# Kernel tuning notes

Measured on AMD Instinct MI355X. Metric: run time of the kernel, lower is better.

## Reference

```python
import jax, jax.numpy as jnp
import numpy as np

B, S, D = 4, 2048, 1024
H, K = 16, 64
NUM_WINDOW = 8
LN_EPS = 1e-3  # keras LayerNormalization default epsilon


def _mha(x, Wq, bq, Wk, bk, Wv, bv, Wo, bo):
    # x: [b, s, D]; Wq/Wk/Wv: [D, H, K]; Wo: [H, K, D]
    q = jnp.einsum('bsd,dhk->bshk', x, Wq) + bq
    k = jnp.einsum('bsd,dhk->bshk', x, Wk) + bk
    v = jnp.einsum('bsd,dhk->bshk', x, Wv) + bv
    scores = jnp.einsum('bqhk,bshk->bhqs', q, k) / jnp.sqrt(jnp.asarray(K, q.dtype))
    attn = jax.nn.softmax(scores, axis=-1)
    o = jnp.einsum('bhqs,bshk->bqhk', attn, v)
    return jnp.einsum('bqhk,hkd->bqd', o, Wo) + bo


def setup_inputs() -> dict:
    key = jax.random.key(0)
    ks = jax.random.split(key, 20)
    sc = 0.02
    def proj(k):
        return jax.random.normal(k, (D, H, K), jnp.float32) * sc
    inp = {
        'x': jax.random.normal(ks[0], (B, S, D), jnp.float32),
        # global MHA params
        'gWq': proj(ks[1]), 'gbq': jnp.zeros((H, K), jnp.float32),
        'gWk': proj(ks[2]), 'gbk': jnp.zeros((H, K), jnp.float32),
        'gWv': proj(ks[3]), 'gbv': jnp.zeros((H, K), jnp.float32),
        'gWo': jax.random.normal(ks[4], (H, K, D), jnp.float32) * sc,
        'gbo': jnp.zeros((D,), jnp.float32),
        # local MHA params (shared across all windows)
        'lWq': proj(ks[5]), 'lbq': jnp.zeros((H, K), jnp.float32),
        'lWk': proj(ks[6]), 'lbk': jnp.zeros((H, K), jnp.float32),
        'lWv': proj(ks[7]), 'lbv': jnp.zeros((H, K), jnp.float32),
        'lWo': jax.random.normal(ks[8], (H, K, D), jnp.float32) * sc,
        'lbo': jnp.zeros((D,), jnp.float32),
        # layernorm params
        'gamma': jnp.ones((D,), jnp.float32),
        'beta': jnp.zeros((D,), jnp.float32),
    }
    return inp


def reference(x, gWq, gbq, gWk, gbk, gWv, gbv, gWo, gbo,
              lWq, lbq, lWk, lbk, lWv, lbv, lWo, lbo, gamma, beta):
    # global full self-attention
    g_out = _mha(x, gWq, gbq, gWk, gbk, gWv, gbv, gWo, gbo)
    # local windowed self-attention: split seq into NUM_WINDOW blocks; all
    # windows share the same local_mha weights, so fold windows into batch.
    w = S // NUM_WINDOW
    xw = x.reshape(B * NUM_WINDOW, w, D)
    l_out = _mha(xw, lWq, lbq, lWk, lbk, lWv, lbv, lWo, lbo).reshape(B, S, D)
    # residual add of all three streams, then layernorm
    y = x + g_out + l_out
    mu = jnp.mean(y, axis=-1, keepdims=True)
    var = jnp.mean(jnp.square(y - mu), axis=-1, keepdims=True)
    return (y - mu) * jax.lax.rsqrt(var + LN_EPS) * gamma + beta
```

## Files before the change

### kernel.cpp

```cpp
#include <hip/hip_runtime.h>
#include <hip/hip_bf16.h>
#include <type_traits>

using bf16 = __hip_bfloat16;
typedef __bf16 bf16x8 __attribute__((ext_vector_type(8)));
typedef float f32x4 __attribute__((ext_vector_type(4)));
typedef float f32x16 __attribute__((ext_vector_type(16)));
typedef unsigned short u16x8 __attribute__((ext_vector_type(8)));
typedef unsigned int u32;
typedef unsigned int u32x4 __attribute__((ext_vector_type(4)));

#define LOG2E 1.4426950408889634f

static __device__ __forceinline__ unsigned short f2bf_bits(float f) {
  bf16 h = __float2bfloat16(f);
  return __builtin_bit_cast(unsigned short, h);
}

__global__ __launch_bounds__(256) void wtr_kernel(const float* __restrict__ W,
                                                  bf16* __restrict__ out,
                                                  int out_ld, int r_off) {
  __shared__ float tile[32][33];
  int tx = threadIdx.x & 31, ty = threadIdx.x >> 5;
  int c0 = blockIdx.x * 32, r0 = blockIdx.y * 32;
#pragma unroll
  for (int i = 0; i < 4; ++i)
    tile[ty + i * 8][tx] = W[(size_t)(r0 + ty + i * 8) * 1024 + c0 + tx];
  __syncthreads();
#pragma unroll
  for (int i = 0; i < 4; ++i) {
    int cr = ty + i * 8;
    out[(size_t)(c0 + cr) * out_ld + r_off + r0 + tx] = __float2bfloat16(tile[tx][cr]);
  }
}

__global__ void biascat_kernel(const float* gbq, const float* gbk, const float* gbv,
                               const float* lbq, const float* lbk, const float* lbv,
                               const float* gbo, const float* lbo,
                               float* bqkv, float* bo) {
  int i = blockIdx.x * 256 + threadIdx.x;
  if (i < 1024) {
    bqkv[i] = gbq[i];
    bqkv[1024 + i] = gbk[i];
    bqkv[2048 + i] = gbv[i];
    bqkv[3072 + i] = lbq[i];
    bqkv[4096 + i] = lbk[i];
    bqkv[5120 + i] = lbv[i];
    bo[i] = gbo[i] + lbo[i];
  }
}

__global__ __launch_bounds__(256) void castx_kernel(const float* __restrict__ x,
                                                    unsigned short* __restrict__ xb) {
  size_t i = (size_t)blockIdx.x * 256 + threadIdx.x;
  float4 v = reinterpret_cast<const float4*>(x)[i];
  ushort4 o = make_ushort4(f2bf_bits(v.x), f2bf_bits(v.y), f2bf_bits(v.z), f2bf_bits(v.w));
  reinterpret_cast<ushort4*>(xb)[i] = o;
}

template <typename OutT>
__global__ __launch_bounds__(256) void gemm_bt_kernel(
    const bf16* __restrict__ A, const bf16* __restrict__ Bt,
    OutT* __restrict__ C, const float* __restrict__ bias,
    int M, int N, int Kd) {
  __shared__ unsigned short lA[128 * 64];
  __shared__ unsigned short lB[128 * 64];
  const int tid = threadIdx.x;
  const int lane = tid & 63;
  const int wv = tid >> 6;
  const int g = lane >> 4, r15 = lane & 15;
  const int nbx = N >> 7;
  const int nwg = gridDim.x;
  const int bid = blockIdx.x;
  const int wg = (bid & 7) * (nwg >> 3) + (bid >> 3);
  const int tR = (wg / nbx) << 7;
  const int tC = (wg % nbx) << 7;
  const int wr = wv >> 1, wc = wv & 1;

  f32x4 acc[4][4] = {};

  const int srow = lane >> 3;
  const int scol = ((lane & 7) ^ (lane >> 3)) << 3;

  const bf16* Ab = A + (size_t)tR * Kd;
  const bf16* Bb = Bt + (size_t)tC * Kd;

  const int nk = Kd >> 6;
  for (int kt = 0; kt < nk; ++kt) {
    const int k0 = kt << 6;
#pragma unroll
    for (int i = 0; i < 4; ++i) {
      const int c = i * 4 + wv;
      const bf16* gA = Ab + (size_t)(c * 8 + srow) * Kd + (k0 + scol);
      __builtin_amdgcn_global_load_lds(
          (const __attribute__((address_space(1))) unsigned int*)gA,
          (__attribute__((address_space(3))) unsigned int*)&lA[c * 512], 16, 0, 0);
      const bf16* gB = Bb + (size_t)(c * 8 + srow) * Kd + (k0 + scol);
      __builtin_amdgcn_global_load_lds(
          (const __attribute__((address_space(1))) unsigned int*)gB,
          (__attribute__((address_space(3))) unsigned int*)&lB[c * 512], 16, 0, 0);
    }
    __syncthreads();
#pragma unroll
    for (int kk = 0; kk < 2; ++kk) {
      bf16x8 af[4], bfr[4];
#pragma unroll
      for (int m = 0; m < 4; ++m) {
        int row = (wr << 6) + (m << 4) + r15;
        int byt = row * 128 + (((kk << 6) + (g << 4)) ^ ((row & 7) << 4));
        af[m] = *reinterpret_cast<const bf16x8*>((const char*)lA + byt);
      }
#pragma unroll
      for (int n = 0; n < 4; ++n) {
        int row = (wc << 6) + (n << 4) + r15;
        int byt = row * 128 + (((kk << 6) + (g << 4)) ^ ((row & 7) << 4));
        bfr[n] = *reinterpret_cast<const bf16x8*>((const char*)lB + byt);
      }
#pragma unroll
      for (int m = 0; m < 4; ++m)
#pragma unroll
        for (int n = 0; n < 4; ++n)
          acc[m][n] = __builtin_amdgcn_mfma_f32_16x16x32_bf16(af[m], bfr[n], acc[m][n], 0, 0, 0);
    }
    __syncthreads();
  }

#pragma unroll
  for (int n = 0; n < 4; ++n) {
    const int col = tC + (wc << 6) + (n << 4) + r15;
    const float bv = bias ? bias[col] : 0.0f;
#pragma unroll
    for (int m = 0; m < 4; ++m) {
      const int row0 = tR + (wr << 6) + (m << 4) + (g << 2);
#pragma unroll
      for (int j = 0; j < 4; ++j) {
        float v = acc[m][n][j] + bv;
        if constexpr (std::is_same<OutT, float>::value)
          C[(size_t)(row0 + j) * N + col] = v;
        else
          C[(size_t)(row0 + j) * N + col] = __float2bfloat16(v);
      }
    }
  }
}

__global__ __launch_bounds__(256) void vtr_kernel(const bf16* __restrict__ qkv,
                                                  bf16* __restrict__ vt, int colOff) {
  __shared__ unsigned short t[64][72];
  const int tid = threadIdx.x;
  const int s0 = blockIdx.x * 64, h = blockIdx.y, b = blockIdx.z;
  const int sr = tid >> 3, d0 = (tid & 7) * 8;
  const bf16* src = qkv + colOff + h * 64;
#pragma unroll
  for (int p = 0; p < 2; ++p) {
    int s = sr + p * 32;
    u16x8 v = *reinterpret_cast<const u16x8*>(src + (size_t)(b * 2048 + s0 + s) * 6144 + d0);
    *reinterpret_cast<u16x8*>(&t[s][d0]) = v;
  }
  __syncthreads();
  bf16* dst = vt + (size_t)((b * 16 + h) * 64) * 2048 + s0;
#pragma unroll
  for (int p = 0; p < 2; ++p) {
    int d = sr + p * 32;
    u16x8 o;
#pragma unroll
    for (int i = 0; i < 8; ++i) o[i] = t[d0 + i][d];
    *reinterpret_cast<u16x8*>(dst + (size_t)d * 2048 + d0) = o;
  }
}

__global__ __launch_bounds__(256, 3) void attn_kernel(
    const bf16* __restrict__ qkv, const bf16* __restrict__ vt,
    bf16* __restrict__ outp, int qOff, int kOff, int oOff, int isLocal) {
  __shared__ unsigned short lK[2][64 * 64];
  __shared__ unsigned short lV[2][64 * 64];
  const int ldq = 6144;
  const int tid = threadIdx.x, lane = tid & 63, wv = tid >> 6;
  const int q31 = lane & 31, hi = lane >> 5;
  const int qb = blockIdx.x, h = blockIdx.y, b = blockIdx.z;
  const int q0 = qb * 128 + wv * 32;

  const int srow = lane >> 3;
  const int scol = ((lane & 7) ^ (lane >> 3)) << 3;

  const bf16* qp = qkv + (size_t)(b * 2048 + q0 + q31) * ldq + qOff + h * 64 + hi * 8;
  bf16x8 qf0 = *reinterpret_cast<const bf16x8*>(qp);
  bf16x8 qf1 = *reinterpret_cast<const bf16x8*>(qp + 16);
  bf16x8 qf2 = *reinterpret_cast<const bf16x8*>(qp + 32);
  bf16x8 qf3 = *reinterpret_cast<const bf16x8*>(qp + 48);

  const int t0 = isLocal ? ((qb >> 1) << 2) : 0;
  const int nt = isLocal ? 4 : 32;

  const bf16* Kb = qkv + kOff + h * 64;
  const bf16* Vb = vt + (size_t)((b * 16 + h) * 64) * 2048;

  auto stage = [&](int t, int buf) {
    const int krow0 = b * 2048 + t * 64;
#pragma unroll
    for (int i = 0; i < 2; ++i) {
      const int c = i * 4 + wv;
      const int row = c * 8 + srow;
      const bf16* gK = Kb + (size_t)(krow0 + row) * ldq + scol;
      __builtin_amdgcn_global_load_lds(
          (const __attribute__((address_space(1))) unsigned int*)gK,
          (__attribute__((address_space(3))) unsigned int*)&lK[buf][c * 512], 16, 0, 0);
      const bf16* gV = Vb + (size_t)row * 2048 + t * 64 + scol;
      __builtin_amdgcn_global_load_lds(
          (const __attribute__((address_space(1))) unsigned int*)gV,
          (__attribute__((address_space(3))) unsigned int*)&lV[buf][c * 512], 16, 0, 0);
    }
  };

  float mrun = -1e30f, lrun = 0.f;
  f32x16 accO0 = {}, accO1 = {};
  const float C8 = 0.125f * LOG2E;

  stage(t0, 0);
  for (int tt = 0; tt < nt; ++tt) {
    const int buf = tt & 1;
    __syncthreads();
    if (tt + 1 < nt) stage(t0 + tt + 1, buf ^ 1);

    f32x16 s0 = {}, s1 = {};
    const char* lkb = (const char*)&lK[buf][0];
#pragma unroll
    for (int kap = 0; kap < 4; ++kap) {
      bf16x8 qf = kap == 0 ? qf0 : kap == 1 ? qf1 : kap == 2 ? qf2 : qf3;
      {
        const int row = q31;
        bf16x8 kf = *reinterpret_cast<const bf16x8*>(
            lkb + row * 128 + ((kap * 32 + hi * 16) ^ ((row & 7) << 4)));
        s0 = __builtin_amdgcn_mfma_f32_32x32x16_bf16(kf, qf, s0, 0, 0, 0);
      }
      {
        const int row = 32 + q31;
        bf16x8 kf = *reinterpret_cast<const bf16x8*>(
            lkb + row * 128 + ((kap * 32 + hi * 16) ^ ((row & 7) << 4)));
        s1 = __builtin_amdgcn_mfma_f32_32x32x16_bf16(kf, qf, s1, 0, 0, 0);
      }
    }

    float m2 = s0[0];
#pragma unroll
    for (int i = 1; i < 16; ++i) m2 = fmaxf(m2, s0[i]);
#pragma unroll
    for (int i = 0; i < 16; ++i) m2 = fmaxf(m2, s1[i]);
    m2 = fmaxf(m2, __shfl_xor(m2, 32));
    if (__any(m2 > mrun + 64.0f)) {
      float mn = fmaxf(mrun, m2);
      float ascl = exp2f((mrun - mn) * C8);
      mrun = mn;
      lrun *= ascl;
      accO0 *= ascl;
      accO1 *= ascl;
    }
    const float nm = -mrun * C8;
    float rs = 0.f;
#pragma unroll
    for (int i = 0; i < 16; ++i) { s0[i] = exp2f(fmaf(s0[i], C8, nm)); rs += s0[i]; }
#pragma unroll
    for (int i = 0; i < 16; ++i) { s1[i] = exp2f(fmaf(s1[i], C8, nm)); rs += s1[i]; }
    rs += __shfl_xor(rs, 32);
    lrun += rs;

    u32 W0[8], W1[8];
#pragma unroll
    for (int m = 0; m < 4; ++m)
#pragma unroll
      for (int u = 0; u < 2; ++u) {
        W0[m * 2 + u] = (u32)f2bf_bits(s0[m * 4 + 2 * u]) |
                        ((u32)f2bf_bits(s0[m * 4 + 2 * u + 1]) << 16);
        W1[m * 2 + u] = (u32)f2bf_bits(s1[m * 4 + 2 * u]) |
                        ((u32)f2bf_bits(s1[m * 4 + 2 * u + 1]) << 16);
      }

    const char* lvb = (const char*)&lV[buf][0];
#define PV_BLOCK(Wb, KAP)                                                          \
  {                                                                                \
    u32 w0 = Wb[(((KAP) & 1) * 2) * 2 + 0], w1 = Wb[(((KAP) & 1) * 2) * 2 + 1];    \
    u32 w2 = Wb[(((KAP) & 1) * 2 + 1) * 2 + 0], w3 = Wb[(((KAP) & 1) * 2 + 1) * 2 + 1]; \
    asm("v_permlane32_swap_b32 %0, %1" : "+v"(w0), "+v"(w2));                      \
    asm("v_permlane32_swap_b32 %0, %1" : "+v"(w1), "+v"(w3));                      \
    bf16x8 pa = __builtin_bit_cast(bf16x8, (u32x4){w0, w1, w2, w3});               \
    {                                                                              \
      const int row = q31;                                                         \
      bf16x8 vf = *reinterpret_cast<const bf16x8*>(                                \
          lvb + row * 128 + (((KAP) * 32 + hi * 16) ^ ((row & 7) << 4)));          \
      accO0 = __builtin_amdgcn_mfma_f32_32x32x16_bf16(vf, pa, accO0, 0, 0, 0);     \
    }                                                                              \
    {                                                                              \
      const int row = 32 + q31;                                                    \
      bf16x8 vf = *reinterpret_cast<const bf16x8*>(                                \
          lvb + row * 128 + (((KAP) * 32 + hi * 16) ^ ((row & 7) << 4)));          \
      accO1 = __builtin_amdgcn_mfma_f32_32x32x16_bf16(vf, pa, accO1, 0, 0, 0);     \
    }                                                                              \
  }
    PV_BLOCK(W0, 0)
    PV_BLOCK(W0, 1)
    PV_BLOCK(W1, 2)
    PV_BLOCK(W1, 3)
#undef PV_BLOCK
  }

  const float inv = 1.0f / lrun;
  bf16* orow = outp + (size_t)(b * 2048 + q0 + q31) * 2048 + oOff + h * 64;
#pragma unroll
  for (int rg = 0; rg < 4; ++rg) {
    const int d0 = 8 * rg + 4 * hi;
    ushort4 o0 = make_ushort4(f2bf_bits(accO0[4 * rg + 0] * inv), f2bf_bits(accO0[4 * rg + 1] * inv),
                              f2bf_bits(accO0[4 * rg + 2] * inv), f2bf_bits(accO0[4 * rg + 3] * inv));
    *reinterpret_cast<ushort4*>(orow + d0) = o0;
    ushort4 o1 = make_ushort4(f2bf_bits(accO1[4 * rg + 0] * inv), f2bf_bits(accO1[4 * rg + 1] * inv),
                              f2bf_bits(accO1[4 * rg + 2] * inv), f2bf_bits(accO1[4 * rg + 3] * inv));
    *reinterpret_cast<ushort4*>(orow + 32 + d0) = o1;
  }
}

__global__ __launch_bounds__(256) void ln_kernel(const float* __restrict__ x,
                                                 const float* __restrict__ ygl,
                                                 const float* __restrict__ gamma,
                                                 const float* __restrict__ beta,
                                                 float* __restrict__ out) {
  const int row = blockIdx.x, t = threadIdx.x, lane = t & 63, wv = t >> 6;
  __shared__ float red[8];
  const float4* xr = reinterpret_cast<const float4*>(x + (size_t)row * 1024);
  const float4* yr = reinterpret_cast<const float4*>(ygl + (size_t)row * 1024);
  float4 a = xr[t], c = yr[t];
  float y0 = a.x + c.x, y1 = a.y + c.y, y2 = a.z + c.z, y3 = a.w + c.w;
  float s = y0 + y1 + y2 + y3;
#pragma unroll
  for (int o = 32; o; o >>= 1) s += __shfl_down(s, o);
  if (!lane) red[wv] = s;
  __syncthreads();
  float mu = (red[0] + red[1] + red[2] + red[3]) * (1.f / 1024.f);
  float d0 = y0 - mu, d1 = y1 - mu, d2 = y2 - mu, d3 = y3 - mu;
  float q = d0 * d0 + d1 * d1 + d2 * d2 + d3 * d3;
#pragma unroll
  for (int o = 32; o; o >>= 1) q += __shfl_down(q, o);
  if (!lane) red[4 + wv] = q;
  __syncthreads();
  float var = (red[4] + red[5] + red[6] + red[7]) * (1.f / 1024.f);
  float r = rsqrtf(var + 1e-3f);
  float4 gm = reinterpret_cast<const float4*>(gamma)[t];
  float4 bt = reinterpret_cast<const float4*>(beta)[t];
  float4 o4;
  o4.x = d0 * r * gm.x + bt.x;
  o4.y = d1 * r * gm.y + bt.y;
  o4.z = d2 * r * gm.z + bt.z;
  o4.w = d3 * r * gm.w + bt.w;
  reinterpret_cast<float4*>(out + (size_t)row * 1024)[t] = o4;
}

extern "C" void kernel_launch(void* const* d_in, const int* in_sizes, int n_in,
                              void* d_out, int out_size, void* d_ws, size_t ws_size,
                              hipStream_t stream) {
  const float* x = (const float*)d_in[0];
  const float* gWq = (const float*)d_in[1];
  const float* gbq = (const float*)d_in[2];
  const float* gWk = (const float*)d_in[3];
  const float* gbk = (const float*)d_in[4];
  const float* gWv = (const float*)d_in[5];
  const float* gbv = (const float*)d_in[6];
  const float* gWo = (const float*)d_in[7];
  const float* gbo = (const float*)d_in[8];
  const float* lWq = (const float*)d_in[9];
  const float* lbq = (const float*)d_in[10];
  const float* lWk = (const float*)d_in[11];
  const float* lbk = (const float*)d_in[12];
  const float* lWv = (const float*)d_in[13];
  const float* lbv = (const float*)d_in[14];
  const float* lWo = (const float*)d_in[15];
  const float* lbo = (const float*)d_in[16];
  const float* gamma = (const float*)d_in[17];
  const float* beta = (const float*)d_in[18];
  float* out = (float*)d_out;

  char* ws = (char*)d_ws;
  size_t off = 0;
  auto alloc = [&](size_t bytes) {
    void* p = ws + off;
    off += (bytes + 255) & ~(size_t)255;
    return p;
  };
  bf16* xb = (bf16*)alloc((size_t)8192 * 1024 * 2);
  bf16* Wt = (bf16*)alloc((size_t)6144 * 1024 * 2);
  bf16* WoT = (bf16*)alloc((size_t)1024 * 2048 * 2);
  float* bQKV = (float*)alloc(6144 * 4);
  float* bO = (float*)alloc(1024 * 4);
  bf16* QKV = (bf16*)alloc((size_t)8192 * 6144 * 2);
  bf16* Vtg = (bf16*)alloc((size_t)64 * 64 * 2048 * 2);
  bf16* Vtl = (bf16*)alloc((size_t)64 * 64 * 2048 * 2);
  bf16* OgOl = (bf16*)alloc((size_t)8192 * 2048 * 2);
  float* ygl = (float*)QKV;

  dim3 blk(256);
  wtr_kernel<<<dim3(32, 32), blk, 0, stream>>>(gWq, Wt + (size_t)0 * 1024 * 1024, 1024, 0);
  wtr_kernel<<<dim3(32, 32), blk, 0, stream>>>(gWk, Wt + (size_t)1 * 1024 * 1024, 1024, 0);
  wtr_kernel<<<dim3(32, 32), blk, 0, stream>>>(gWv, Wt + (size_t)2 * 1024 * 1024, 1024, 0);
  wtr_kernel<<<dim3(32, 32), blk, 0, stream>>>(lWq, Wt + (size_t)3 * 1024 * 1024, 1024, 0);
  wtr_kernel<<<dim3(32, 32), blk, 0, stream>>>(lWk, Wt + (size_t)4 * 1024 * 1024, 1024, 0);
  wtr_kernel<<<dim3(32, 32), blk, 0, stream>>>(lWv, Wt + (size_t)5 * 1024 * 1024, 1024, 0);
  wtr_kernel<<<dim3(32, 32), blk, 0, stream>>>(gWo, WoT, 2048, 0);
  wtr_kernel<<<dim3(32, 32), blk, 0, stream>>>(lWo, WoT, 2048, 1024);
  biascat_kernel<<<dim3(4), blk, 0, stream>>>(gbq, gbk, gbv, lbq, lbk, lbv, gbo, lbo, bQKV, bO);
  castx_kernel<<<dim3(8192), blk, 0, stream>>>(x, (unsigned short*)xb);
  gemm_bt_kernel<bf16><<<dim3(64 * 48), blk, 0, stream>>>(xb, Wt, QKV, bQKV, 8192, 6144, 1024);
  vtr_kernel<<<dim3(32, 16, 4), blk, 0, stream>>>(QKV, Vtg, 2048);
  vtr_kernel<<<dim3(32, 16, 4), blk, 0, stream>>>(QKV, Vtl, 5120);
  attn_kernel<<<dim3(16, 16, 4), blk, 0, stream>>>(QKV, Vtg, OgOl, 0, 1024, 0, 0);
  attn_kernel<<<dim3(16, 16, 4), blk, 0, stream>>>(QKV, Vtl, OgOl, 3072, 4096, 1024, 1);
  gemm_bt_kernel<float><<<dim3(64 * 8), blk, 0, stream>>>(OgOl, WoT, ygl, bO, 8192, 1024, 2048);
  ln_kernel<<<dim3(8192), blk, 0, stream>>>(x, ygl, gamma, beta, out);
}
```

Measured before the change: 513.3 us.

## Move softmax row-sum to MFMA, tree-reduce max, packed bf16 converts

```diff
diff --git a/kernel.cpp b/kernel.cpp
--- a/kernel.cpp
+++ b/kernel.cpp
@@ -212,18 +212,21 @@
     }
   };
 
-  float mrun = -1e30f, lrun = 0.f;
-  f32x16 accO0 = {}, accO1 = {};
+  float mrun = -1e30f;
+  f32x16 accO0 = {}, accO1 = {}, accL = {};
   const float C8 = 0.125f * LOG2E;
+  const u32x4 onep = {0x3F803F80u, 0x3F803F80u, 0x3F803F80u, 0x3F803F80u};
+  const bf16x8 onesA = __builtin_bit_cast(bf16x8, onep);
 
   stage(t0, 0);
-  for (int tt = 0; tt < nt; ++tt) {
-    const int buf = tt & 1;
+
+  auto body = [&](int tt, auto bufc) {
+    constexpr int BUF = decltype(bufc)::value;
     __syncthreads();
-    if (tt + 1 < nt) stage(t0 + tt + 1, buf ^ 1);
+    if (tt + 1 < nt) stage(t0 + tt + 1, BUF ^ 1);
 
     f32x16 s0 = {}, s1 = {};
-    const char* lkb = (const char*)&lK[buf][0];
+    const char* lkb = (const char*)&lK[BUF][0];
 #pragma unroll
     for (int kap = 0; kap < 4; ++kap) {
       bf16x8 qf = kap == 0 ? qf0 : kap == 1 ? qf1 : kap == 2 ? qf2 : qf3;
@@ -241,41 +244,42 @@
       }
     }
 
-    float m2 = s0[0];
-#pragma unroll
-    for (int i = 1; i < 16; ++i) m2 = fmaxf(m2, s0[i]);
-#pragma unroll
-    for (int i = 0; i < 16; ++i) m2 = fmaxf(m2, s1[i]);
-    m2 = fmaxf(m2, __shfl_xor(m2, 32));
+    float t16[16];
+#pragma unroll
+    for (int i = 0; i < 16; ++i) t16[i] = fmaxf(s0[i], s1[i]);
+#pragma unroll
+    for (int st = 8; st; st >>= 1)
+#pragma unroll
+      for (int i = 0; i < st; ++i) t16[i] = fmaxf(t16[i], t16[i + st]);
+    float m2 = fmaxf(t16[0], __shfl_xor(t16[0], 32));
     if (__any(m2 > mrun + 64.0f)) {
       float mn = fmaxf(mrun, m2);
       float ascl = exp2f((mrun - mn) * C8);
       mrun = mn;
-      lrun *= ascl;
       accO0 *= ascl;
       accO1 *= ascl;
+      accL *= ascl;
     }
     const float nm = -mrun * C8;
-    float rs = 0.f;
-#pragma unroll
-    for (int i = 0; i < 16; ++i) { s0[i] = exp2f(fmaf(s0[i], C8, nm)); rs += s0[i]; }
-#pragma unroll
-    for (int i = 0; i < 16; ++i) { s1[i] = exp2f(fmaf(s1[i], C8, nm)); rs += s1[i]; }
-    rs += __shfl_xor(rs, 32);
-    lrun += rs;
+#pragma unroll
+    for (int i = 0; i < 16; ++i) s0[i] = exp2f(fmaf(s0[i], C8, nm));
+#pragma unroll
+    for (int i = 0; i < 16; ++i) s1[i] = exp2f(fmaf(s1[i], C8, nm));
 
     u32 W0[8], W1[8];
 #pragma unroll
     for (int m = 0; m < 4; ++m)
 #pragma unroll
       for (int u = 0; u < 2; ++u) {
-        W0[m * 2 + u] = (u32)f2bf_bits(s0[m * 4 + 2 * u]) |
-                        ((u32)f2bf_bits(s0[m * 4 + 2 * u + 1]) << 16);
-        W1[m * 2 + u] = (u32)f2bf_bits(s1[m * 4 + 2 * u]) |
-                        ((u32)f2bf_bits(s1[m * 4 + 2 * u + 1]) << 16);
-      }
-
-    const char* lvb = (const char*)&lV[buf][0];
+        asm("v_cvt_pk_bf16_f32 %0, %1, %2"
+            : "=v"(W0[m * 2 + u])
+            : "v"(s0[m * 4 + 2 * u]), "v"(s0[m * 4 + 2 * u + 1]));
+        asm("v_cvt_pk_bf16_f32 %0, %1, %2"
+            : "=v"(W1[m * 2 + u])
+            : "v"(s1[m * 4 + 2 * u]), "v"(s1[m * 4 + 2 * u + 1]));
+      }
+
+    const char* lvb = (const char*)&lV[BUF][0];
 #define PV_BLOCK(Wb, KAP)                                                          \
   {                                                                                \
     u32 w0 = Wb[(((KAP) & 1) * 2) * 2 + 0], w1 = Wb[(((KAP) & 1) * 2) * 2 + 1];    \
@@ -295,15 +299,21 @@
           lvb + row * 128 + (((KAP) * 32 + hi * 16) ^ ((row & 7) << 4)));          \
       accO1 = __builtin_amdgcn_mfma_f32_32x32x16_bf16(vf, pa, accO1, 0, 0, 0);     \
     }                                                                              \
+    accL = __builtin_amdgcn_mfma_f32_32x32x16_bf16(onesA, pa, accL, 0, 0, 0);      \
   }
     PV_BLOCK(W0, 0)
     PV_BLOCK(W0, 1)
     PV_BLOCK(W1, 2)
     PV_BLOCK(W1, 3)
 #undef PV_BLOCK
-  }
-
-  const float inv = 1.0f / lrun;
+  };
+
+  for (int tt = 0; tt < nt; tt += 2) {
+    body(tt, std::integral_constant<int, 0>{});
+    body(tt + 1, std::integral_constant<int, 1>{});
+  }
+
+  const float inv = 1.0f / accL[0];
   bf16* orow = outp + (size_t)(b * 2048 + q0 + q31) * 2048 + oOff + h * 64;
 #pragma unroll
   for (int rg = 0; rg < 4; ++rg) {
```

New measurement: 516.0 us. Within noise of the previous version (+0.5%).
